# Kernel tuning notes

Measured on AMD Instinct MI355X. Metric: run time of the kernel, lower is better.

## Reference

```python
import jax, jax.numpy as jnp
import numpy as np

N, E, H = 50000, 400000, 128
BN_EPS = 1e-5


def _bn_relu(x, g, b):
    # BatchNorm1d in training mode: biased batch variance
    m = x.mean(axis=0)
    v = jnp.var(x, axis=0)
    return jax.nn.relu((x - m) * (g / jnp.sqrt(v + BN_EPS)) + b)


def _mlp(x, W1, G1, B1, W2, G2, B2):
    # Linear(no bias) -> BN -> ReLU -> Linear(no bias) -> BN -> ReLU
    h = _bn_relu(x @ W1, G1, B1)
    return _bn_relu(h @ W2, G2, B2)


def setup_inputs() -> dict:
    key = jax.random.key(0)
    ks = jax.random.split(key, 16)
    node_rep = jax.random.normal(ks[0], (N, H), jnp.float32)
    edge_rep = jax.random.normal(ks[1], (E, H), jnp.float32)
    src = jax.random.randint(ks[2], (E,), 0, N, jnp.int32)
    dst = jax.random.randint(ks[3], (E,), 0, N, jnp.int32)
    deg = np.bincount(np.asarray(src), minlength=N) + np.bincount(np.asarray(dst), minlength=N)
    degree = jnp.asarray(deg, jnp.float32)

    def lin(k, fi, fo):
        return jax.random.normal(k, (fi, fo), jnp.float32) / np.sqrt(fi)

    def bn(k, f):
        kg, kb = jax.random.split(k)
        return (1.0 + 0.01 * jax.random.normal(kg, (f,), jnp.float32),
                0.01 * jax.random.normal(kb, (f,), jnp.float32))

    inp = dict(node_rep=node_rep, edge_rep=edge_rep, degree=degree,
               src=src, dst=dst,
               eps1=jnp.zeros((1,), jnp.float32), eps2=jnp.zeros((1,), jnp.float32))
    specs = {'n': H, 'e0': 2 * H, 'e1': H, 'e2': H}
    i = 4
    for name, fin in specs.items():
        W1 = lin(ks[i], fin, 2 * H); G1, B1 = bn(ks[i + 1], 2 * H)
        W2 = lin(ks[i + 2], 2 * H, H); G2, B2 = bn(ks[i + 3], H)
        i += 3
        inp.update({f'{name}W1': W1, f'{name}G1': G1, f'{name}B1': B1,
                    f'{name}W2': W2, f'{name}G2': G2, f'{name}B2': B2})
    return inp


def reference(node_rep, edge_rep, degree, src, dst, eps1, eps2,
              nW1, nG1, nB1, nW2, nG2, nB2,
              e0W1, e0G1, e0B1, e0W2, e0G2, e0B2,
              e1W1, e1G1, e1B1, e1W2, e1G2, e1B2,
              e2W1, e2G1, e2B1, e2W2, e2G2, e2B2):
    # node -> edge gather: sum endpoint node features per edge
    node2edge = node_rep[src] + node_rep[dst]                      # [E,H]
    # edge -> edge gather: per-node sum of incident edges, summed over endpoints
    S = (jax.ops.segment_sum(edge_rep, src, num_segments=N)
         + jax.ops.segment_sum(edge_rep, dst, num_segments=N))     # [N,H]
    edge2edge = S[src] + S[dst]                                    # [E,H]

    edge_new = _mlp(jnp.concatenate([node2edge, edge2edge], axis=-1),
                    e0W1, e0G1, e0B1, e0W2, e0G2, e0B2)
    edge_new = (1.0 + eps1) * edge_rep + edge_new                  # GIN-style residual

    edge_out = _mlp(edge_new, e1W1, e1G1, e1B1, e1W2, e1G2, e1B2)

    edge2node_e = _mlp(edge_new, e2W1, e2G1, e2B1, e2W2, e2G2, e2B2)
    # edge -> node gather: sum incident edge messages at each node
    edge2node = (jax.ops.segment_sum(edge2node_e, src, num_segments=N)
                 + jax.ops.segment_sum(edge2node_e, dst, num_segments=N))

    node_in = (1.0 + eps2 - degree[:, None]) * node_rep + edge2node
    node_out = _mlp(node_in, nW1, nG1, nB1, nW2, nG2, nB2)
    return (node_out, edge_out)
```

## Files before the change

kernel.cpp:

```cpp
#include <hip/hip_runtime.h>
#include <hip/hip_bf16.h>
#include <cstdint>

#define EDGES 400000
#define NODES 50000
#define HDIM  128

typedef unsigned short u16;
typedef __bf16 bf16x8 __attribute__((ext_vector_type(8)));
typedef float  f32x4  __attribute__((ext_vector_type(4)));

__device__ __forceinline__ float bf2f(u16 u) {
    union { uint32_t i; float f; } w; w.i = ((uint32_t)u) << 16; return w.f;
}
__device__ __forceinline__ u16 f2bf(float f) {
    union { float f; uint32_t i; } w; w.f = f;
    uint32_t x = w.i;
    uint32_t r = (x + 0x7fffu + ((x >> 16) & 1u)) >> 16;
    return (u16)r;
}

__global__ void wt_convert(const float* __restrict__ W, u16* __restrict__ Wt,
                           int K, int Nout) {
    int idx = blockIdx.x * 256 + threadIdx.x;
    if (idx < K * Nout) {
        int n = idx / K, k = idx - n * K;
        Wt[idx] = f2bf(W[(size_t)k * Nout + n]);
    }
}

__global__ void scatter_S(const float* __restrict__ edge_rep,
                          const int* __restrict__ src, const int* __restrict__ dst,
                          float* __restrict__ S) {
    size_t stride = (size_t)gridDim.x * blockDim.x;
    for (size_t i = (size_t)blockIdx.x * blockDim.x + threadIdx.x;
         i < (size_t)EDGES * HDIM; i += stride) {
        int e = (int)(i >> 7), h = (int)(i & 127);
        float v = edge_rep[i];
        atomicAdd(&S[(size_t)src[e] * HDIM + h], v);
        atomicAdd(&S[(size_t)dst[e] * HDIM + h], v);
    }
}

__global__ void build_x0(const float* __restrict__ node_rep, const float* __restrict__ S,
                         const int* __restrict__ src, const int* __restrict__ dst,
                         u16* __restrict__ X0) {
    size_t stride = (size_t)gridDim.x * blockDim.x;
    for (size_t i = (size_t)blockIdx.x * blockDim.x + threadIdx.x;
         i < (size_t)EDGES * HDIM; i += stride) {
        int e = (int)(i >> 7), h = (int)(i & 127);
        size_t so = (size_t)src[e] * HDIM + h, doo = (size_t)dst[e] * HDIM + h;
        X0[(size_t)e * 256 + h]       = f2bf(node_rep[so] + node_rep[doo]);
        X0[(size_t)e * 256 + 128 + h] = f2bf(S[so] + S[doo]);
    }
}

template<int K>
__global__ __launch_bounds__(256) void gemm_bn(
    const u16* __restrict__ A, const u16* __restrict__ Wt,
    u16* __restrict__ Out, float* __restrict__ stats, int M, int Nout)
{
    __shared__ u16 Al[128][72];
    __shared__ u16 Bl[128][72];
    const int tid  = threadIdx.x;
    const int lane = tid & 63;
    const int w    = tid >> 6;
    const int wrow = w >> 1, wcol = w & 1;
    const int mrow0 = blockIdx.x * 128;
    const int ncol0 = blockIdx.y * 128;
    f32x4 acc[4][4] = {};

    const int srow = tid >> 3;
    const int sc8  = (tid & 7) * 8;

    for (int k0 = 0; k0 < K; k0 += 64) {
        if (k0) __syncthreads();
        #pragma unroll
        for (int p = 0; p < 4; ++p) {
            int row  = srow + p * 32;
            int grow = mrow0 + row;
            uint4 va = make_uint4(0u, 0u, 0u, 0u);
            if (grow < M)
                va = *reinterpret_cast<const uint4*>(&A[(size_t)grow * K + k0 + sc8]);
            *reinterpret_cast<uint4*>(&Al[row][sc8]) = va;
            uint4 vb = *reinterpret_cast<const uint4*>(&Wt[(size_t)(ncol0 + row) * K + k0 + sc8]);
            *reinterpret_cast<uint4*>(&Bl[row][sc8]) = vb;
        }
        __syncthreads();
        #pragma unroll
        for (int kk = 0; kk < 64; kk += 32) {
            const int lr = lane & 15;
            const int kc = kk + (lane >> 4) * 8;
            bf16x8 af[4], bfr[4];
            #pragma unroll
            for (int m = 0; m < 4; ++m)
                af[m] = *reinterpret_cast<const bf16x8*>(&Al[wrow * 64 + m * 16 + lr][kc]);
            #pragma unroll
            for (int n = 0; n < 4; ++n)
                bfr[n] = *reinterpret_cast<const bf16x8*>(&Bl[wcol * 64 + n * 16 + lr][kc]);
            #pragma unroll
            for (int m = 0; m < 4; ++m)
                #pragma unroll
                for (int n = 0; n < 4; ++n)
                    acc[m][n] = __builtin_amdgcn_mfma_f32_16x16x32_bf16(
                        af[m], bfr[n], acc[m][n], 0, 0, 0);
        }
    }

    const int lr = lane & 15, lq = lane >> 4;
    #pragma unroll
    for (int m = 0; m < 4; ++m) {
        #pragma unroll
        for (int n = 0; n < 4; ++n) {
            int col = ncol0 + wcol * 64 + n * 16 + lr;
            #pragma unroll
            for (int i = 0; i < 4; ++i) {
                int row = mrow0 + wrow * 64 + m * 16 + lq * 4 + i;
                if (row < M)
                    Out[(size_t)row * Nout + col] = f2bf(acc[m][n][i]);
            }
        }
    }
    #pragma unroll
    for (int n = 0; n < 4; ++n) {
        float s = 0.f, q = 0.f;
        #pragma unroll
        for (int m = 0; m < 4; ++m)
            #pragma unroll
            for (int i = 0; i < 4; ++i) { float v = acc[m][n][i]; s += v; q += v * v; }
        s += __shfl_xor(s, 16); s += __shfl_xor(s, 32);
        q += __shfl_xor(q, 16); q += __shfl_xor(q, 32);
        if (lq == 0) {
            int col = ncol0 + wcol * 64 + n * 16 + lr;
            atomicAdd(&stats[col], s);
            atomicAdd(&stats[Nout + col], q);
        }
    }
}

__global__ void bn_finalize(const float* __restrict__ stats, const float* __restrict__ G,
                            const float* __restrict__ Bi, float* __restrict__ scsh,
                            int Nout, float invM) {
    int j = threadIdx.x;
    if (j < Nout) {
        float mean = stats[j] * invM;
        float var  = stats[Nout + j] * invM - mean * mean;
        float sc   = G[j] / sqrtf(var + 1e-5f);
        scsh[j]        = sc;
        scsh[Nout + j] = Bi[j] - mean * sc;
    }
}

__global__ void bn_apply(u16* __restrict__ Hh, const float* __restrict__ scsh,
                         int mask, int Nout, size_t count) {
    size_t stride = (size_t)gridDim.x * blockDim.x;
    for (size_t i = (size_t)blockIdx.x * blockDim.x + threadIdx.x; i < count; i += stride) {
        int c = (int)(i & mask);
        float v = bf2f(Hh[i]);
        Hh[i] = f2bf(fmaxf(v * scsh[c] + scsh[Nout + c], 0.f));
    }
}

__global__ void edge_new_k(const float* __restrict__ edge_rep, const u16* __restrict__ H2,
                           const float* __restrict__ scsh, const float* __restrict__ eps1,
                           u16* __restrict__ EN) {
    float e1 = 1.0f + eps1[0];
    size_t stride = (size_t)gridDim.x * blockDim.x;
    for (size_t i = (size_t)blockIdx.x * blockDim.x + threadIdx.x;
         i < (size_t)EDGES * HDIM; i += stride) {
        int h = (int)(i & 127);
        float m = fmaxf(bf2f(H2[i]) * scsh[h] + scsh[128 + h], 0.f);
        EN[i] = f2bf(e1 * edge_rep[i] + m);
    }
}

__global__ void edge_out_k(const u16* __restrict__ H4, const float* __restrict__ scsh,
                           float* __restrict__ out) {
    size_t stride = (size_t)gridDim.x * blockDim.x;
    for (size_t i = (size_t)blockIdx.x * blockDim.x + threadIdx.x;
         i < (size_t)EDGES * HDIM; i += stride) {
        int h = (int)(i & 127);
        out[i] = fmaxf(bf2f(H4[i]) * scsh[h] + scsh[128 + h], 0.f);
    }
}

__global__ void scatter_e2n(const u16* __restrict__ H6, const float* __restrict__ scsh,
                            const int* __restrict__ src, const int* __restrict__ dst,
                            float* __restrict__ An) {
    size_t stride = (size_t)gridDim.x * blockDim.x;
    for (size_t i = (size_t)blockIdx.x * blockDim.x + threadIdx.x;
         i < (size_t)EDGES * HDIM; i += stride) {
        int e = (int)(i >> 7), h = (int)(i & 127);
        float m = fmaxf(bf2f(H6[i]) * scsh[h] + scsh[128 + h], 0.f);
        atomicAdd(&An[(size_t)src[e] * HDIM + h], m);
        atomicAdd(&An[(size_t)dst[e] * HDIM + h], m);
    }
}

__global__ void node_in_k(const float* __restrict__ node_rep, const float* __restrict__ An,
                          const float* __restrict__ degree, const float* __restrict__ eps2,
                          u16* __restrict__ NI) {
    float e2 = 1.0f + eps2[0];
    size_t stride = (size_t)gridDim.x * blockDim.x;
    for (size_t i = (size_t)blockIdx.x * blockDim.x + threadIdx.x;
         i < (size_t)NODES * HDIM; i += stride) {
        int n = (int)(i >> 7);
        NI[i] = f2bf((e2 - degree[n]) * node_rep[i] + An[i]);
    }
}

__global__ void node_out_k(const u16* __restrict__ H8, const float* __restrict__ scsh,
                           float* __restrict__ out) {
    size_t stride = (size_t)gridDim.x * blockDim.x;
    for (size_t i = (size_t)blockIdx.x * blockDim.x + threadIdx.x;
         i < (size_t)NODES * HDIM; i += stride) {
        int h = (int)(i & 127);
        out[i] = fmaxf(bf2f(H8[i]) * scsh[h] + scsh[128 + h], 0.f);
    }
}

extern "C" void kernel_launch(void* const* d_in, const int* in_sizes, int n_in,
                              void* d_out, int out_size, void* d_ws, size_t ws_size,
                              hipStream_t stream) {
    const float* node_rep = (const float*)d_in[0];
    const float* edge_rep = (const float*)d_in[1];
    const float* degree   = (const float*)d_in[2];
    const int*   src      = (const int*)d_in[3];
    const int*   dst      = (const int*)d_in[4];
    const float* eps1     = (const float*)d_in[5];
    const float* eps2     = (const float*)d_in[6];
    const float* nW1  = (const float*)d_in[7];
    const float* nG1  = (const float*)d_in[8];
    const float* nB1  = (const float*)d_in[9];
    const float* nW2  = (const float*)d_in[10];
    const float* nG2  = (const float*)d_in[11];
    const float* nB2  = (const float*)d_in[12];
    const float* e0W1 = (const float*)d_in[13];
    const float* e0G1 = (const float*)d_in[14];
    const float* e0B1 = (const float*)d_in[15];
    const float* e0W2 = (const float*)d_in[16];
    const float* e0G2 = (const float*)d_in[17];
    const float* e0B2 = (const float*)d_in[18];
    const float* e1W1 = (const float*)d_in[19];
    const float* e1G1 = (const float*)d_in[20];
    const float* e1B1 = (const float*)d_in[21];
    const float* e1W2 = (const float*)d_in[22];
    const float* e1G2 = (const float*)d_in[23];
    const float* e1B2 = (const float*)d_in[24];
    const float* e2W1 = (const float*)d_in[25];
    const float* e2G1 = (const float*)d_in[26];
    const float* e2B1 = (const float*)d_in[27];
    const float* e2W2 = (const float*)d_in[28];
    const float* e2G2 = (const float*)d_in[29];
    const float* e2B2 = (const float*)d_in[30];

    size_t off = 0;
    auto alloc = [&](size_t bytes) -> void* {
        void* p = (char*)d_ws + off;
        off += (bytes + 255) & ~(size_t)255;
        return p;
    };
    u16*   BUF_A = (u16*)alloc((size_t)EDGES * 256 * 2);
    u16*   BUF_B = (u16*)alloc((size_t)EDGES * 256 * 2);
    u16*   BUF_C = (u16*)alloc((size_t)EDGES * 128 * 2);
    u16*   BUF_D = (u16*)alloc((size_t)EDGES * 128 * 2);
    float* S     = (float*)alloc((size_t)NODES * 128 * 4);
    float* An    = (float*)alloc((size_t)NODES * 128 * 4);
    u16*   NI    = (u16*)alloc((size_t)NODES * 128 * 2);
    u16*   H7    = (u16*)alloc((size_t)NODES * 256 * 2);
    u16*   H8    = (u16*)alloc((size_t)NODES * 128 * 2);
    u16* Wt_e0_1 = (u16*)alloc(256 * 256 * 2);
    u16* Wt_e0_2 = (u16*)alloc(128 * 256 * 2);
    u16* Wt_e1_1 = (u16*)alloc(256 * 128 * 2);
    u16* Wt_e1_2 = (u16*)alloc(128 * 256 * 2);
    u16* Wt_e2_1 = (u16*)alloc(256 * 128 * 2);
    u16* Wt_e2_2 = (u16*)alloc(128 * 256 * 2);
    u16* Wt_n_1  = (u16*)alloc(256 * 128 * 2);
    u16* Wt_n_2  = (u16*)alloc(128 * 256 * 2);
    float* stats = (float*)alloc(8 * 512 * 4);
    float* scsh  = (float*)alloc(8 * 512 * 4);
    if (off > ws_size) return;

    hipMemsetAsync(S,     0, (size_t)NODES * 128 * 4, stream);
    hipMemsetAsync(An,    0, (size_t)NODES * 128 * 4, stream);
    hipMemsetAsync(stats, 0, 8 * 512 * 4, stream);

    const int EB = 8192;
    const float invE = 1.0f / (float)EDGES;
    const float invN = 1.0f / (float)NODES;
    const dim3 gE2(3125, 2), gE1(3125, 1), gN2(391, 2), gN1(391, 1);

    wt_convert<<<(256 * 256 + 255) / 256, 256, 0, stream>>>(e0W1, Wt_e0_1, 256, 256);
    wt_convert<<<(128 * 256 + 255) / 256, 256, 0, stream>>>(e0W2, Wt_e0_2, 256, 128);
    wt_convert<<<(256 * 128 + 255) / 256, 256, 0, stream>>>(e1W1, Wt_e1_1, 128, 256);
    wt_convert<<<(128 * 256 + 255) / 256, 256, 0, stream>>>(e1W2, Wt_e1_2, 256, 128);
    wt_convert<<<(256 * 128 + 255) / 256, 256, 0, stream>>>(e2W1, Wt_e2_1, 128, 256);
    wt_convert<<<(128 * 256 + 255) / 256, 256, 0, stream>>>(e2W2, Wt_e2_2, 256, 128);
    wt_convert<<<(256 * 128 + 255) / 256, 256, 0, stream>>>(nW1, Wt_n_1, 128, 256);
    wt_convert<<<(128 * 256 + 255) / 256, 256, 0, stream>>>(nW2, Wt_n_2, 256, 128);

    scatter_S<<<EB, 256, 0, stream>>>(edge_rep, src, dst, S);
    build_x0<<<EB, 256, 0, stream>>>(node_rep, S, src, dst, BUF_A);

    gemm_bn<256><<<gE2, 256, 0, stream>>>(BUF_A, Wt_e0_1, BUF_B, stats + 0 * 512, EDGES, 256);
    bn_finalize<<<1, 256, 0, stream>>>(stats + 0 * 512, e0G1, e0B1, scsh + 0 * 512, 256, invE);
    bn_apply<<<EB, 256, 0, stream>>>(BUF_B, scsh + 0 * 512, 255, 256, (size_t)EDGES * 256);
    gemm_bn<256><<<gE1, 256, 0, stream>>>(BUF_B, Wt_e0_2, BUF_C, stats + 1 * 512, EDGES, 128);
    bn_finalize<<<1, 256, 0, stream>>>(stats + 1 * 512, e0G2, e0B2, scsh + 1 * 512, 128, invE);
    edge_new_k<<<EB, 256, 0, stream>>>(edge_rep, BUF_C, scsh + 1 * 512, eps1, BUF_D);

    gemm_bn<128><<<gE2, 256, 0, stream>>>(BUF_D, Wt_e1_1, BUF_A, stats + 2 * 512, EDGES, 256);
    bn_finalize<<<1, 256, 0, stream>>>(stats + 2 * 512, e1G1, e1B1, scsh + 2 * 512, 256, invE);
    bn_apply<<<EB, 256, 0, stream>>>(BUF_A, scsh + 2 * 512, 255, 256, (size_t)EDGES * 256);
    gemm_bn<256><<<gE1, 256, 0, stream>>>(BUF_A, Wt_e1_2, BUF_C, stats + 3 * 512, EDGES, 128);
    bn_finalize<<<1, 256, 0, stream>>>(stats + 3 * 512, e1G2, e1B2, scsh + 3 * 512, 128, invE);
    edge_out_k<<<EB, 256, 0, stream>>>(BUF_C, scsh + 3 * 512,
                                       (float*)d_out + (size_t)NODES * HDIM);

    gemm_bn<128><<<gE2, 256, 0, stream>>>(BUF_D, Wt_e2_1, BUF_B, stats + 4 * 512, EDGES, 256);
    bn_finalize<<<1, 256, 0, stream>>>(stats + 4 * 512, e2G1, e2B1, scsh + 4 * 512, 256, invE);
    bn_apply<<<EB, 256, 0, stream>>>(BUF_B, scsh + 4 * 512, 255, 256, (size_t)EDGES * 256);
    gemm_bn<256><<<gE1, 256, 0, stream>>>(BUF_B, Wt_e2_2, BUF_C, stats + 5 * 512, EDGES, 128);
    bn_finalize<<<1, 256, 0, stream>>>(stats + 5 * 512, e2G2, e2B2, scsh + 5 * 512, 128, invE);
    scatter_e2n<<<EB, 256, 0, stream>>>(BUF_C, scsh + 5 * 512, src, dst, An);

    node_in_k<<<EB, 256, 0, stream>>>(node_rep, An, degree, eps2, NI);
    gemm_bn<128><<<gN2, 256, 0, stream>>>(NI, Wt_n_1, H7, stats + 6 * 512, NODES, 256);
    bn_finalize<<<1, 256, 0, stream>>>(stats + 6 * 512, nG1, nB1, scsh + 6 * 512, 256, invN);
    bn_apply<<<EB, 256, 0, stream>>>(H7, scsh + 6 * 512, 255, 256, (size_t)NODES * 256);
    gemm_bn<256><<<gN1, 256, 0, stream>>>(H7, Wt_n_2, H8, stats + 7 * 512, NODES, 128);
    bn_finalize<<<1, 256, 0, stream>>>(stats + 7 * 512, nG2, nB2, scsh + 7 * 512, 128, invN);
    node_out_k<<<EB, 256, 0, stream>>>(H8, scsh + 7 * 512, (float*)d_out);
}
```

Before: 3.263 ms.

## Fuse BN+ReLU into next GEMM's A-load and vectorize elementwise kernels

Removes the separate bn_apply passes by applying the first BatchNorm affine and ReLU while loading A tiles into shared memory in the second GEMM of each MLP. This saves one full read and write of each 256-wide hidden activation. The elementwise kernels (build_x0, edge_new, output affine, node_in) are also rewritten to handle 8 elements per thread with float4/uint4 accesses and packed bf16 conversion. The cost is extra ALU work inside the GEMM load path, done once per N-block.

```diff
diff --git a/kernel.cpp b/kernel.cpp
--- a/kernel.cpp
+++ b/kernel.cpp
@@ -18,6 +18,32 @@
     uint32_t x = w.i;
     uint32_t r = (x + 0x7fffu + ((x >> 16) & 1u)) >> 16;
     return (u16)r;
+}
+__device__ __forceinline__ uint32_t pk_bf16(float lo, float hi) {
+    union { float f; uint32_t i; } a, b; a.f = lo; b.f = hi;
+    uint32_t rl = (a.i + 0x7fffu + ((a.i >> 16) & 1u)) >> 16;
+    uint32_t rh = (b.i + 0x7fffu + ((b.i >> 16) & 1u)) & 0xffff0000u;
+    return rl | rh;
+}
+__device__ __forceinline__ void unpk2(uint32_t h2, float& lo, float& hi) {
+    union { uint32_t i; float f; } a, b;
+    a.i = h2 << 16; b.i = h2 & 0xffff0000u; lo = a.f; hi = b.f;
+}
+__device__ __forceinline__ uint32_t bnrelu2(uint32_t h2, float scl, float sch,
+                                            float shl_, float shh) {
+    float lo, hi; unpk2(h2, lo, hi);
+    return pk_bf16(fmaxf(fmaf(lo, scl, shl_), 0.f),
+                   fmaxf(fmaf(hi, sch, shh), 0.f));
+}
+__device__ __forceinline__ uint4 bnrelu8(uint4 v, const float* __restrict__ sc,
+                                         const float* __restrict__ sh) {
+    float4 s0 = *(const float4*)sc, s1 = *(const float4*)(sc + 4);
+    float4 t0 = *(const float4*)sh, t1 = *(const float4*)(sh + 4);
+    v.x = bnrelu2(v.x, s0.x, s0.y, t0.x, t0.y);
+    v.y = bnrelu2(v.y, s0.z, s0.w, t0.z, t0.w);
+    v.z = bnrelu2(v.z, s1.x, s1.y, t1.x, t1.y);
+    v.w = bnrelu2(v.w, s1.z, s1.w, t1.z, t1.w);
+    return v;
 }
 
 __global__ void wt_convert(const float* __restrict__ W, u16* __restrict__ Wt,
@@ -42,23 +68,39 @@
     }
 }
 
-__global__ void build_x0(const float* __restrict__ node_rep, const float* __restrict__ S,
-                         const int* __restrict__ src, const int* __restrict__ dst,
-                         u16* __restrict__ X0) {
-    size_t stride = (size_t)gridDim.x * blockDim.x;
-    for (size_t i = (size_t)blockIdx.x * blockDim.x + threadIdx.x;
-         i < (size_t)EDGES * HDIM; i += stride) {
-        int e = (int)(i >> 7), h = (int)(i & 127);
-        size_t so = (size_t)src[e] * HDIM + h, doo = (size_t)dst[e] * HDIM + h;
-        X0[(size_t)e * 256 + h]       = f2bf(node_rep[so] + node_rep[doo]);
-        X0[(size_t)e * 256 + 128 + h] = f2bf(S[so] + S[doo]);
-    }
-}
-
-template<int K>
+__global__ void build_x0_v(const float* __restrict__ node_rep, const float* __restrict__ S,
+                           const int* __restrict__ src, const int* __restrict__ dst,
+                           u16* __restrict__ X0) {
+    size_t stride = (size_t)gridDim.x * blockDim.x;
+    for (size_t t = (size_t)blockIdx.x * blockDim.x + threadIdx.x;
+         t < (size_t)EDGES * 16; t += stride) {
+        int e  = (int)(t >> 4);
+        int h8 = (int)(t & 15) * 8;
+        size_t so = (size_t)src[e] * HDIM + h8;
+        size_t dv = (size_t)dst[e] * HDIM + h8;
+        float4 a0 = *(const float4*)&node_rep[so], a1 = *(const float4*)&node_rep[so + 4];
+        float4 b0 = *(const float4*)&node_rep[dv], b1 = *(const float4*)&node_rep[dv + 4];
+        float4 c0 = *(const float4*)&S[so],        c1 = *(const float4*)&S[so + 4];
+        float4 d0 = *(const float4*)&S[dv],        d1 = *(const float4*)&S[dv + 4];
+        uint4 o1, o2;
+        o1.x = pk_bf16(a0.x + b0.x, a0.y + b0.y);
+        o1.y = pk_bf16(a0.z + b0.z, a0.w + b0.w);
+        o1.z = pk_bf16(a1.x + b1.x, a1.y + b1.y);
+        o1.w = pk_bf16(a1.z + b1.z, a1.w + b1.w);
+        o2.x = pk_bf16(c0.x + d0.x, c0.y + d0.y);
+        o2.y = pk_bf16(c0.z + d0.z, c0.w + d0.w);
+        o2.z = pk_bf16(c1.x + d1.x, c1.y + d1.y);
+        o2.w = pk_bf16(c1.z + d1.z, c1.w + d1.w);
+        *(uint4*)&X0[(size_t)e * 256 + h8]       = o1;
+        *(uint4*)&X0[(size_t)e * 256 + 128 + h8] = o2;
+    }
+}
+
+template<int K, bool FUSE>
 __global__ __launch_bounds__(256) void gemm_bn(
     const u16* __restrict__ A, const u16* __restrict__ Wt,
-    u16* __restrict__ Out, float* __restrict__ stats, int M, int Nout)
+    u16* __restrict__ Out, float* __restrict__ stats, int M, int Nout,
+    const float* __restrict__ fsc)
 {
     __shared__ u16 Al[128][72];
     __shared__ u16 Bl[128][72];
@@ -80,8 +122,11 @@
             int row  = srow + p * 32;
             int grow = mrow0 + row;
             uint4 va = make_uint4(0u, 0u, 0u, 0u);
-            if (grow < M)
+            if (grow < M) {
                 va = *reinterpret_cast<const uint4*>(&A[(size_t)grow * K + k0 + sc8]);
+                if (FUSE)
+                    va = bnrelu8(va, &fsc[k0 + sc8], &fsc[K + k0 + sc8]);
+            }
             *reinterpret_cast<uint4*>(&Al[row][sc8]) = va;
             uint4 vb = *reinterpret_cast<const uint4*>(&Wt[(size_t)(ncol0 + row) * K + k0 + sc8]);
             *reinterpret_cast<uint4*>(&Bl[row][sc8]) = vb;
@@ -151,36 +196,54 @@
     }
 }
 
-__global__ void bn_apply(u16* __restrict__ Hh, const float* __restrict__ scsh,
-                         int mask, int Nout, size_t count) {
-    size_t stride = (size_t)gridDim.x * blockDim.x;
-    for (size_t i = (size_t)blockIdx.x * blockDim.x + threadIdx.x; i < count; i += stride) {
-        int c = (int)(i & mask);
-        float v = bf2f(Hh[i]);
-        Hh[i] = f2bf(fmaxf(v * scsh[c] + scsh[Nout + c], 0.f));
-    }
-}
-
-__global__ void edge_new_k(const float* __restrict__ edge_rep, const u16* __restrict__ H2,
+__global__ void edge_new_v(const float* __restrict__ edge_rep, const u16* __restrict__ H2,
                            const float* __restrict__ scsh, const float* __restrict__ eps1,
                            u16* __restrict__ EN) {
     float e1 = 1.0f + eps1[0];
     size_t stride = (size_t)gridDim.x * blockDim.x;
-    for (size_t i = (size_t)blockIdx.x * blockDim.x + threadIdx.x;
-         i < (size_t)EDGES * HDIM; i += stride) {
-        int h = (int)(i & 127);
-        float m = fmaxf(bf2f(H2[i]) * scsh[h] + scsh[128 + h], 0.f);
-        EN[i] = f2bf(e1 * edge_rep[i] + m);
-    }
-}
-
-__global__ void edge_out_k(const u16* __restrict__ H4, const float* __restrict__ scsh,
-                           float* __restrict__ out) {
-    size_t stride = (size_t)gridDim.x * blockDim.x;
-    for (size_t i = (size_t)blockIdx.x * blockDim.x + threadIdx.x;
-         i < (size_t)EDGES * HDIM; i += stride) {
-        int h = (int)(i & 127);
-        out[i] = fmaxf(bf2f(H4[i]) * scsh[h] + scsh[128 + h], 0.f);
+    for (size_t t = (size_t)blockIdx.x * blockDim.x + threadIdx.x;
+         t < (size_t)EDGES * 16; t += stride) {
+        size_t base = t * 8;
+        int h8 = (int)(t & 15) * 8;
+        uint4 h = *(const uint4*)&H2[base];
+        h = bnrelu8(h, &scsh[h8], &scsh[128 + h8]);
+        float4 r0 = *(const float4*)&edge_rep[base];
+        float4 r1 = *(const float4*)&edge_rep[base + 4];
+        float m0, m1, m2, m3, m4, m5, m6, m7;
+        unpk2(h.x, m0, m1); unpk2(h.y, m2, m3);
+        unpk2(h.z, m4, m5); unpk2(h.w, m6, m7);
+        uint4 o;
+        o.x = pk_bf16(fmaf(e1, r0.x, m0), fmaf(e1, r0.y, m1));
+        o.y = pk_bf16(fmaf(e1, r0.z, m2), fmaf(e1, r0.w, m3));
+        o.z = pk_bf16(fmaf(e1, r1.x, m4), fmaf(e1, r1.y, m5));
+        o.w = pk_bf16(fmaf(e1, r1.z, m6), fmaf(e1, r1.w, m7));
+        *(uint4*)&EN[base] = o;
+    }
+}
+
+__global__ void affine_out_v(const u16* __restrict__ H, const float* __restrict__ scsh,
+                             float* __restrict__ out, size_t t16) {
+    size_t stride = (size_t)gridDim.x * blockDim.x;
+    for (size_t t = (size_t)blockIdx.x * blockDim.x + threadIdx.x; t < t16; t += stride) {
+        size_t base = t * 8;
+        int h8 = (int)(t & 15) * 8;
+        uint4 h = *(const uint4*)&H[base];
+        float4 s0 = *(const float4*)&scsh[h8],       s1 = *(const float4*)&scsh[h8 + 4];
+        float4 t0 = *(const float4*)&scsh[128 + h8], t1 = *(const float4*)&scsh[128 + h8 + 4];
+        float v0, v1, v2, v3, v4, v5, v6, v7;
+        unpk2(h.x, v0, v1); unpk2(h.y, v2, v3);
+        unpk2(h.z, v4, v5); unpk2(h.w, v6, v7);
+        float4 o0, o1;
+        o0.x = fmaxf(fmaf(v0, s0.x, t0.x), 0.f);
+        o0.y = fmaxf(fmaf(v1, s0.y, t0.y), 0.f);
+        o0.z = fmaxf(fmaf(v2, s0.z, t0.z), 0.f);
+        o0.w = fmaxf(fmaf(v3, s0.w, t0.w), 0.f);
+        o1.x = fmaxf(fmaf(v4, s1.x, t1.x), 0.f);
+        o1.y = fmaxf(fmaf(v5, s1.y, t1.y), 0.f);
+        o1.z = fmaxf(fmaf(v6, s1.z, t1.z), 0.f);
+        o1.w = fmaxf(fmaf(v7, s1.w, t1.w), 0.f);
+        *(float4*)&out[base]     = o0;
+        *(float4*)&out[base + 4] = o1;
     }
 }
 
@@ -197,25 +260,24 @@
     }
 }
 
-__global__ void node_in_k(const float* __restrict__ node_rep, const float* __restrict__ An,
+__global__ void node_in_v(const float* __restrict__ node_rep, const float* __restrict__ An,
                           const float* __restrict__ degree, const float* __restrict__ eps2,
                           u16* __restrict__ NI) {
     float e2 = 1.0f + eps2[0];
     size_t stride = (size_t)gridDim.x * blockDim.x;
-    for (size_t i = (size_t)blockIdx.x * blockDim.x + threadIdx.x;
-         i < (size_t)NODES * HDIM; i += stride) {
-        int n = (int)(i >> 7);
-        NI[i] = f2bf((e2 - degree[n]) * node_rep[i] + An[i]);
-    }
-}
-
-__global__ void node_out_k(const u16* __restrict__ H8, const float* __restrict__ scsh,
-                           float* __restrict__ out) {
-    size_t stride = (size_t)gridDim.x * blockDim.x;
-    for (size_t i = (size_t)blockIdx.x * blockDim.x + threadIdx.x;
-         i < (size_t)NODES * HDIM; i += stride) {
-        int h = (int)(i & 127);
-        out[i] = fmaxf(bf2f(H8[i]) * scsh[h] + scsh[128 + h], 0.f);
+    for (size_t t = (size_t)blockIdx.x * blockDim.x + threadIdx.x;
+         t < (size_t)NODES * 16; t += stride) {
+        int n = (int)(t >> 4);
+        size_t base = t * 8;
+        float c = e2 - degree[n];
+        float4 r0 = *(const float4*)&node_rep[base], r1 = *(const float4*)&node_rep[base + 4];
+        float4 a0 = *(const float4*)&An[base],       a1 = *(const float4*)&An[base + 4];
+        uint4 o;
+        o.x = pk_bf16(fmaf(c, r0.x, a0.x), fmaf(c, r0.y, a0.y));
+        o.y = pk_bf16(fmaf(c, r0.z, a0.z), fmaf(c, r0.w, a0.w));
+        o.z = pk_bf16(fmaf(c, r1.x, a1.x), fmaf(c, r1.y, a1.y));
+        o.w = pk_bf16(fmaf(c, r1.z, a1.z), fmaf(c, r1.w, a1.w));
+        *(uint4*)&NI[base] = o;
     }
 }
 
@@ -285,7 +347,9 @@
     hipMemsetAsync(An,    0, (size_t)NODES * 128 * 4, stream);
     hipMemsetAsync(stats, 0, 8 * 512 * 4, stream);
 
-    const int EB = 8192;
+    const int EB  = 8192;
+    const int EV  = 4096;
+    const int NV  = 3125;
     const float invE = 1.0f / (float)EDGES;
     const float invN = 1.0f / (float)NODES;
     const dim3 gE2(3125, 2), gE1(3125, 1), gN2(391, 2), gN1(391, 1);
@@ -300,35 +364,33 @@
     wt_convert<<<(128 * 256 + 255) / 256, 256, 0, stream>>>(nW2, Wt_n_2, 256, 128);
 
     scatter_S<<<EB, 256, 0, stream>>>(edge_rep, src, dst, S);
-    build_x0<<<EB, 256, 0, stream>>>(node_rep, S, src, dst, BUF_A);
-
-    gemm_bn<256><<<gE2, 256, 0, stream>>>(BUF_A, Wt_e0_1, BUF_B, stats + 0 * 512, EDGES, 256);
+    build_x0_v<<<EV, 256, 0, stream>>>(node_rep, S, src, dst, BUF_A);
+
+    gemm_bn<256, false><<<gE2, 256, 0, stream>>>(BUF_A, Wt_e0_1, BUF_B, stats + 0 * 512, EDGES, 256, nullptr);
     bn_finalize<<<1, 256, 0, stream>>>(stats + 0 * 512, e0G1, e0B1, scsh + 0 * 512, 256, invE);
-    bn_apply<<<EB, 256, 0, stream>>>(BUF_B, scsh + 0 * 512, 255, 256, (size_t)EDGES * 256);
-    gemm_bn<256><<<gE1, 256, 0, stream>>>(BUF_B, Wt_e0_2, BUF_C, stats + 1 * 512, EDGES, 128);
+    gemm_bn<256, true><<<gE1, 256, 0, stream>>>(BUF_B, Wt_e0_2, BUF_C, stats + 1 * 512, EDGES, 128, scsh + 0 * 512);
     bn_finalize<<<1, 256, 0, stream>>>(stats + 1 * 512, e0G2, e0B2, scsh + 1 * 512, 128, invE);
-    edge_new_k<<<EB, 256, 0, stream>>>(edge_rep, BUF_C, scsh + 1 * 512, eps1, BUF_D);
-
-    gemm_bn<128><<<gE2, 256, 0, stream>>>(BUF_D, Wt_e1_1, BUF_A, stats + 2 * 512, EDGES, 256);
+    edge_new_v<<<EV, 256, 0, stream>>>(edge_rep, BUF_C, scsh + 1 * 512, eps1, BUF_D);
+
+    gemm_bn<128, false><<<gE2, 256, 0, stream>>>(BUF_D, Wt_e1_1, BUF_A, stats + 2 * 512, EDGES, 256, nullptr);
     bn_finalize<<<1, 256, 0, stream>>>(stats + 2 * 512, e1G1, e1B1, scsh + 2 * 512, 256, invE);
-    bn_apply<<<EB, 256, 0, stream>>>(BUF_A, scsh + 2 * 512, 255, 256, (size_t)EDGES * 256);
-    gemm_bn<256><<<gE1, 256, 0, stream>>>(BUF_A, Wt_e1_2, BUF_C, stats + 3 * 512, EDGES, 128);
+    gemm_bn<256, true><<<gE1, 256, 0, stream>>>(BUF_A, Wt_e1_2, BUF_C, stats + 3 * 512, EDGES, 128, scsh + 2 * 512);
     bn_finalize<<<1, 256, 0, stream>>>(stats + 3 * 512, e1G2, e1B2, scsh + 3 * 512, 128, invE);
-    edge_out_k<<<EB, 256, 0, stream>>>(BUF_C, scsh + 3 * 512,
-                                       (float*)d_out + (size_t)NODES * HDIM);
-
-    gemm_bn<128><<<gE2, 256, 0, stream>>>(BUF_D, Wt_e2_1, BUF_B, stats + 4 * 512, EDGES, 256);
+    affine_out_v<<<EV, 256, 0, stream>>>(BUF_C, scsh + 3 * 512,
+                                         (float*)d_out + (size_t)NODES * HDIM,
+                                         (size_t)EDGES * 16);
+
+    gemm_bn<128, false><<<gE2, 256, 0, stream>>>(BUF_D, Wt_e2_1, BUF_B, stats + 4 * 512, EDGES, 256, nullptr);
     bn_finalize<<<1, 256, 0, stream>>>(stats + 4 * 512, e2G1, e2B1, scsh + 4 * 512, 256, invE);
-    bn_apply<<<EB, 256, 0, stream>>>(BUF_B, scsh + 4 * 512, 255, 256, (size_t)EDGES * 256);
-    gemm_bn<256><<<gE1, 256, 0, stream>>>(BUF_B, Wt_e2_2, BUF_C, stats + 5 * 512, EDGES, 128);
+    gemm_bn<256, true><<<gE1, 256, 0, stream>>>(BUF_B, Wt_e2_2, BUF_C, stats + 5 * 512, EDGES, 128, scsh + 4 * 512);
     bn_finalize<<<1, 256, 0, stream>>>(stats + 5 * 512, e2G2, e2B2, scsh + 5 * 512, 128, invE);
     scatter_e2n<<<EB, 256, 0, stream>>>(BUF_C, scsh + 5 * 512, src, dst, An);
 
-    node_in_k<<<EB, 256, 0, stream>>>(node_rep, An, degree, eps2, NI);
-    gemm_bn<128><<<gN2, 256, 0, stream>>>(NI, Wt_n_1, H7, stats + 6 * 512, NODES, 256);
+    node_in_v<<<NV, 256, 0, stream>>>(node_rep, An, degree, eps2, NI);
+    gemm_bn<128, false><<<gN2, 256, 0, stream>>>(NI, Wt_n_1, H7, stats + 6 * 512, NODES, 256, nullptr);
     bn_finalize<<<1, 256, 0, stream>>>(stats + 6 * 512, nG1, nB1, scsh + 6 * 512, 256, invN);
-    bn_apply<<<EB, 256, 0, stream>>>(H7, scsh + 6 * 512, 255, 256, (size_t)NODES * 256);
-    gemm_bn<256><<<gN1, 256, 0, stream>>>(H7, Wt_n_2, H8, stats + 7 * 512, NODES, 128);
+    gemm_bn<256, true><<<gN1, 256, 0, stream>>>(H7, Wt_n_2, H8, stats + 7 * 512, NODES, 128, scsh + 6 * 512);
     bn_finalize<<<1, 256, 0, stream>>>(stats + 7 * 512, nG2, nB2, scsh + 7 * 512, 128, invN);
-    node_out_k<<<EB, 256, 0, stream>>>(H8, scsh + 7 * 512, (float*)d_out);
-}
+    affine_out_v<<<NV, 256, 0, stream>>>(H8, scsh + 7 * 512, (float*)d_out,
+                                         (size_t)NODES * 16);
+}
```

Result: faster. 2.910 ms (-10.8%).
